# Kernel optimization log

Measured on AMD Instinct MI355X. Metric: run time of the kernel, lower is better.

Reference implementation:

```python
import jax, jax.numpy as jnp
import numpy as np

N, E, C, RB, H = 10000, 160000, 64, 8, 64
AVG_NEIGH = 16.0


def _sph(v):
    # component-normalized real spherical harmonics l=1,2,3 of unit vectors v [E,3]
    x, y, z = v[..., 0], v[..., 1], v[..., 2]
    s3, s5, s15 = 3.0 ** 0.5, 5.0 ** 0.5, 15.0 ** 0.5
    y1 = s3 * jnp.stack([x, y, z], -1)  # [E,3]
    y2 = jnp.stack([
        s15 * x * y,
        s15 * y * z,
        0.5 * s5 * (3.0 * z * z - 1.0),
        s15 * x * z,
        0.5 * s15 * (x * x - y * y),
    ], -1)  # [E,5]
    c1 = (35.0 / 8.0) ** 0.5
    c2 = 105.0 ** 0.5
    c3 = (21.0 / 8.0) ** 0.5
    c4 = (7.0 ** 0.5) / 2.0
    y3 = jnp.stack([
        c1 * y * (3.0 * x * x - y * y),
        c2 * x * y * z,
        c3 * y * (5.0 * z * z - 1.0),
        c4 * z * (5.0 * z * z - 3.0),
        c3 * x * (5.0 * z * z - 1.0),
        0.5 * c2 * z * (x * x - y * y),
        c1 * x * (x * x - y * y),
    ], -1)  # [E,7]
    return y1, y2, y3


def setup_inputs() -> dict:
    key = jax.random.key(0)
    ks = jax.random.split(key, 12)
    inp = {
        'vectors': jax.random.normal(ks[0], (E, 3), jnp.float32),
        'node_feats': jax.random.normal(ks[1], (N, C), jnp.float32),
        'radial_embedding': jax.random.normal(ks[2], (E, RB), jnp.float32),
        'W_up': jax.random.normal(ks[3], (C, C), jnp.float32) / np.sqrt(C),
        'mlp_w1': jax.random.normal(ks[4], (RB, H), jnp.float32) / np.sqrt(RB),
        'mlp_w2': jax.random.normal(ks[5], (H, H), jnp.float32) / np.sqrt(H),
        'mlp_w3': jax.random.normal(ks[6], (H, H), jnp.float32) / np.sqrt(H),
        'mlp_w4': jax.random.normal(ks[7], (H, 4 * C), jnp.float32) / np.sqrt(H),
        'W_down': jax.random.normal(ks[8], (4, C, C), jnp.float32) / np.sqrt(C),
        'senders': jax.random.randint(ks[9], (E,), 0, N, jnp.int32),
        'receivers': jax.random.randint(ks[10], (E,), 0, N, jnp.int32),
    }
    return inp


def reference(vectors, node_feats, radial_embedding, W_up, mlp_w1, mlp_w2, mlp_w3, mlp_w4, W_down, senders, receivers):
    n = node_feats.shape[0]
    # linear_up (scalars: plain channel mixing)
    x = node_feats @ W_up                                   # [N,C]
    sf = x[senders]                                         # [E,C] gather
    u = vectors / (jnp.linalg.norm(vectors, axis=-1, keepdims=True) + 1e-12)
    y1, y2, y3 = _sph(u)
    # radial MLP -> per-irrep mixing weights [E, 4C]
    h = jax.nn.silu(radial_embedding @ mlp_w1)
    h = jax.nn.silu(h @ mlp_w2)
    h = jax.nn.silu(h @ mlp_w3)
    mix = h @ mlp_w4
    m0, m1, m2, m3 = jnp.split(mix, 4, axis=-1)             # each [E,C]
    # tensor product of Cx0e with Y_l -> Cx(l), scaled by radial mix
    msg0 = sf * m0                                          # [E,C]
    msg1 = (sf * m1)[:, :, None] * y1[:, None, :]           # [E,C,3]
    msg2 = (sf * m2)[:, :, None] * y2[:, None, :]           # [E,C,5]
    msg3 = (sf * m3)[:, :, None] * y3[:, None, :]           # [E,C,7]
    inv = 1.0 / jnp.sqrt(jnp.asarray(AVG_NEIGH, msg0.dtype))
    seg = lambda m: jax.ops.segment_sum(m, receivers, num_segments=n) * inv
    o0, o1, o2, o3 = seg(msg0), seg(msg1), seg(msg2), seg(msg3)
    # linear_down: per-l channel mixing
    o0 = o0 @ W_down[0]
    o1 = jnp.einsum('ncm,cd->ndm', o1, W_down[1])
    o2 = jnp.einsum('ncm,cd->ndm', o2, W_down[2])
    o3 = jnp.einsum('ncm,cd->ndm', o3, W_down[3])
    return jnp.concatenate([o0, o1.reshape(n, -1), o2.reshape(n, -1), o3.reshape(n, -1)], axis=-1)  # [N, 16C]
```

## Files before the change

### kernel.cpp

```cpp
#include <hip/hip_runtime.h>
#include <math.h>

#define CC 64
typedef _Float16 f16;
typedef _Float16 half8_t __attribute__((ext_vector_type(8)));
typedef float f32x4 __attribute__((ext_vector_type(4)));

__device__ __forceinline__ float silu_f(float v) {
    return v / (1.0f + __expf(-v));
}

__global__ void k_up(const float* __restrict__ nf, const float* __restrict__ Wup,
                     float* __restrict__ x, int N) {
    int tid = blockIdx.x * blockDim.x + threadIdx.x;
    if (tid >= N * CC) return;
    int n = tid >> 6;
    int j = tid & 63;
    const float* nfr = nf + (size_t)n * CC;
    float acc = 0.f;
#pragma unroll
    for (int k = 0; k < CC; ++k) acc += nfr[k] * Wup[k * CC + j];
    x[tid] = acc;
}

__global__ void k_wt(const float* __restrict__ w1, const float* __restrict__ w2,
                     const float* __restrict__ w3, const float* __restrict__ w4,
                     const float* __restrict__ Wd,
                     f16* __restrict__ wT1, f16* __restrict__ wT2,
                     f16* __restrict__ wT3, f16* __restrict__ wT4,
                     float* __restrict__ wpack) {
    int i = blockIdx.x * 256 + threadIdx.x;
    if (i < 2048) {
        int n = i >> 5, k = i & 31;
        wT1[i] = (k < 8) ? (f16)w1[k * 64 + n] : (f16)0.f;
    } else if (i < 6144) {
        int j = i - 2048; int n = j >> 6, k = j & 63;
        wT2[j] = (f16)w2[k * 64 + n];
    } else if (i < 10240) {
        int j = i - 6144; int n = j >> 6, k = j & 63;
        wT3[j] = (f16)w3[k * 64 + n];
    } else if (i < 26624) {
        int j = i - 10240; int l = j >> 12; int r = j & 4095;
        int n = r >> 6, k = r & 63;
        wT4[j] = (f16)w4[k * 256 + l * 64 + n];
    } else if (i < 43008) {
        int j = i - 26624;
        int pos = j >> 2;
        int comp = j & 3;
        wpack[j] = 0.25f * Wd[comp * 4096 + pos];
    }
}

__global__ void k_hist(const int* __restrict__ rcv, int* __restrict__ cnt, int E) {
    int e = blockIdx.x * blockDim.x + threadIdx.x;
    if (e < E) atomicAdd(&cnt[rcv[e]], 1);
}

__global__ __launch_bounds__(1024) void k_scan(const int* __restrict__ cnt,
        int* __restrict__ off, int* __restrict__ cur, int N) {
    __shared__ int wsum[16];
    int t = threadIdx.x;
    int wave = t >> 6, lane = t & 63;
    int per = (N + 1023) >> 10;
    int i0 = t * per;
    int s = 0;
    for (int j = 0; j < per; ++j) {
        int i = i0 + j;
        if (i < N) s += cnt[i];
    }
    int sc = s;
#pragma unroll
    for (int d = 1; d < 64; d <<= 1) {
        int u = __shfl_up(sc, d, 64);
        if (lane >= d) sc += u;
    }
    if (lane == 63) wsum[wave] = sc;
    __syncthreads();
    if (wave == 0) {
        int v = (lane < 16) ? wsum[lane] : 0;
        int s2 = v;
#pragma unroll
        for (int d = 1; d < 16; d <<= 1) {
            int u = __shfl_up(s2, d, 64);
            if (lane >= d) s2 += u;
        }
        if (lane < 16) wsum[lane] = s2;
    }
    __syncthreads();
    int base = ((wave > 0) ? wsum[wave - 1] : 0) + (sc - s);
    int run = base;
    for (int j = 0; j < per; ++j) {
        int i = i0 + j;
        if (i < N) { off[i] = run; cur[i] = run; run += cnt[i]; }
    }
    if (t == 1023) off[N] = run;
}

__global__ void k_fill(const int* __restrict__ rcv, const int* __restrict__ snd,
                       const float* __restrict__ vec, int* __restrict__ cur,
                       int* __restrict__ eid, int* __restrict__ sndp,
                       float* __restrict__ yb, int E) {
    int e = blockIdx.x * blockDim.x + threadIdx.x;
    if (e >= E) return;
    int p = atomicAdd(&cur[rcv[e]], 1);
    eid[p] = e;
    sndp[p] = snd[e];

    float vx = vec[(size_t)e * 3 + 0];
    float vy = vec[(size_t)e * 3 + 1];
    float vz = vec[(size_t)e * 3 + 2];
    float nrm = sqrtf(vx * vx + vy * vy + vz * vz) + 1e-12f;
    float rinv = 1.0f / nrm;
    float ux = vx * rinv, uy = vy * rinv, uz = vz * rinv;

    const float s3 = 1.7320508075688772f;
    const float s5 = 2.2360679774997896f;
    const float s15 = 3.8729833462074170f;
    const float c1 = 2.0916500663351889f;
    const float c2 = 10.246950765959598f;
    const float c3 = 1.6201851746019651f;
    const float c4 = 1.3228756555322954f;

    float zz = uz * uz, xx = ux * ux, yy = uy * uy;
    float4 r0 = {1.0f, s3 * ux, s3 * uy, s3 * uz};
    float4 r1 = {s15 * ux * uy, s15 * uy * uz, 0.5f * s5 * (3.f * zz - 1.f),
                 s15 * ux * uz};
    float4 r2 = {0.5f * s15 * (xx - yy), c1 * uy * (3.f * xx - yy),
                 c2 * ux * uy * uz, c3 * uy * (5.f * zz - 1.f)};
    float4 r3 = {c4 * uz * (5.f * zz - 3.f), c3 * ux * (5.f * zz - 1.f),
                 0.5f * c2 * uz * (xx - yy), c1 * ux * (xx - yy)};
    float* yr = yb + (size_t)p * 16;
    *(float4*)(yr + 0)  = r0;
    *(float4*)(yr + 4)  = r1;
    *(float4*)(yr + 8)  = r2;
    *(float4*)(yr + 12) = r3;
}

__global__ __launch_bounds__(256) void k_mlp(const float* __restrict__ rad,
        const f16* __restrict__ wT1, const f16* __restrict__ wT2,
        const f16* __restrict__ wT3, const f16* __restrict__ wT4,
        const int* __restrict__ eid, const int* __restrict__ sndp,
        const float* __restrict__ x, f16* __restrict__ mixp, int E) {
    __shared__ f16 act[128][72];

    int t = threadIdx.x;
    int e0 = blockIdx.x * 128;
    int lane = t & 63;
    int wid = t >> 6;
    int m0 = wid * 32;
    int fm = lane & 15;
    int q  = lane >> 4;

    const half8_t hz = {0, 0, 0, 0, 0, 0, 0, 0};

    float4 sfa[4], sfb[4];
#pragma unroll
    for (int it = 0; it < 4; ++it) {
        int row = (lane >> 3) + it * 8;
        int ci = e0 + m0 + row;
        int s = (ci < E) ? sndp[ci] : 0;
        const float* xr = x + (size_t)s * 64 + (lane & 7) * 8;
        sfa[it] = *(const float4*)xr;
        sfb[it] = *(const float4*)(xr + 4);
    }

    half8_t a0 = hz, a1 = hz;
    if (q == 0) {
        int ci0 = e0 + m0 + fm;
        if (ci0 < E) {
            int e = eid[ci0];
            float4 p0 = *(const float4*)(rad + (size_t)e * 8);
            float4 p1 = *(const float4*)(rad + (size_t)e * 8 + 4);
            a0 = (half8_t){(f16)p0.x, (f16)p0.y, (f16)p0.z, (f16)p0.w,
                           (f16)p1.x, (f16)p1.y, (f16)p1.z, (f16)p1.w};
        }
        int ci1 = e0 + m0 + 16 + fm;
        if (ci1 < E) {
            int e = eid[ci1];
            float4 p0 = *(const float4*)(rad + (size_t)e * 8);
            float4 p1 = *(const float4*)(rad + (size_t)e * 8 + 4);
            a1 = (half8_t){(f16)p0.x, (f16)p0.y, (f16)p0.z, (f16)p0.w,
                           (f16)p1.x, (f16)p1.y, (f16)p1.z, (f16)p1.w};
        }
    }
#pragma unroll
    for (int nt = 0; nt < 4; ++nt) {
        half8_t b = *(const half8_t*)(wT1 + ((nt * 16 + fm) << 5) + q * 8);
        f32x4 c0 = {0.f, 0.f, 0.f, 0.f};
        c0 = __builtin_amdgcn_mfma_f32_16x16x32_f16(a0, b, c0, 0, 0, 0);
        f32x4 c1 = {0.f, 0.f, 0.f, 0.f};
        c1 = __builtin_amdgcn_mfma_f32_16x16x32_f16(a1, b, c1, 0, 0, 0);
#pragma unroll
        for (int r = 0; r < 4; ++r) {
            act[m0 + q * 4 + r][nt * 16 + fm]      = (f16)silu_f(c0[r]);
            act[m0 + 16 + q * 4 + r][nt * 16 + fm] = (f16)silu_f(c1[r]);
        }
    }

    auto loadA = [&](int mbase, int kc) -> half8_t {
        return *(const half8_t*)&act[mbase + fm][kc + q * 8];
    };

    const f16* wts[2] = {wT2, wT3};
#pragma unroll
    for (int L = 0; L < 2; ++L) {
        const f16* wT = wts[L];
        half8_t a00 = loadA(m0, 0),      a01 = loadA(m0, 32);
        half8_t a10 = loadA(m0 + 16, 0), a11 = loadA(m0 + 16, 32);
#pragma unroll
        for (int nt = 0; nt < 4; ++nt) {
            const f16* wr = wT + ((nt * 16 + fm) << 6);
            half8_t b0 = *(const half8_t*)(wr + q * 8);
            half8_t b1 = *(const half8_t*)(wr + 32 + q * 8);
            f32x4 c0 = {0.f, 0.f, 0.f, 0.f};
            c0 = __builtin_amdgcn_mfma_f32_16x16x32_f16(a00, b0, c0, 0, 0, 0);
            c0 = __builtin_amdgcn_mfma_f32_16x16x32_f16(a01, b1, c0, 0, 0, 0);
            f32x4 c1 = {0.f, 0.f, 0.f, 0.f};
            c1 = __builtin_amdgcn_mfma_f32_16x16x32_f16(a10, b0, c1, 0, 0, 0);
            c1 = __builtin_amdgcn_mfma_f32_16x16x32_f16(a11, b1, c1, 0, 0, 0);
#pragma unroll
            for (int r = 0; r < 4; ++r) {
                act[m0 + q * 4 + r][nt * 16 + fm]      = (f16)silu_f(c0[r]);
                act[m0 + 16 + q * 4 + r][nt * 16 + fm] = (f16)silu_f(c1[r]);
            }
        }
    }

    half8_t A00 = loadA(m0, 0),      A01 = loadA(m0, 32);
    half8_t A10 = loadA(m0 + 16, 0), A11 = loadA(m0 + 16, 32);

#pragma unroll
    for (int l = 0; l < 4; ++l) {
        const f16* wT = wT4 + (l << 12);
#pragma unroll
        for (int nt = 0; nt < 4; ++nt) {
            const f16* wr = wT + ((nt * 16 + fm) << 6);
            half8_t b0 = *(const half8_t*)(wr + q * 8);
            half8_t b1 = *(const half8_t*)(wr + 32 + q * 8);
            f32x4 c0 = {0.f, 0.f, 0.f, 0.f};
            c0 = __builtin_amdgcn_mfma_f32_16x16x32_f16(A00, b0, c0, 0, 0, 0);
            c0 = __builtin_amdgcn_mfma_f32_16x16x32_f16(A01, b1, c0, 0, 0, 0);
            f32x4 c1 = {0.f, 0.f, 0.f, 0.f};
            c1 = __builtin_amdgcn_mfma_f32_16x16x32_f16(A10, b0, c1, 0, 0, 0);
            c1 = __builtin_amdgcn_mfma_f32_16x16x32_f16(A11, b1, c1, 0, 0, 0);
#pragma unroll
            for (int r = 0; r < 4; ++r) {
                act[m0 + q * 4 + r][nt * 16 + fm]      = (f16)c0[r];
                act[m0 + 16 + q * 4 + r][nt * 16 + fm] = (f16)c1[r];
            }
        }
#pragma unroll
        for (int it = 0; it < 4; ++it) {
            int row = (lane >> 3) + it * 8;
            int ci = e0 + m0 + row;
            if (ci < E) {
                half8_t v = *(const half8_t*)&act[m0 + row][(lane & 7) * 8];
                half8_t w;
                w[0] = (f16)((float)v[0] * sfa[it].x);
                w[1] = (f16)((float)v[1] * sfa[it].y);
                w[2] = (f16)((float)v[2] * sfa[it].z);
                w[3] = (f16)((float)v[3] * sfa[it].w);
                w[4] = (f16)((float)v[4] * sfb[it].x);
                w[5] = (f16)((float)v[5] * sfb[it].y);
                w[6] = (f16)((float)v[6] * sfb[it].z);
                w[7] = (f16)((float)v[7] * sfb[it].w);
                *(half8_t*)&mixp[(size_t)ci * 256 + l * 64 + (lane & 7) * 8] = w;
            }
        }
    }
}

__global__ __launch_bounds__(256) void k_gather(
        const f16* __restrict__ mixp, const float* __restrict__ yb,
        const int* __restrict__ off, const f32x4* __restrict__ wpack,
        float* __restrict__ out, int N) {
    __shared__ float sbuf[4][64 * 20];
    __shared__ float ybs[4][16][16];
    int wv = threadIdx.x >> 6;
    int lane = threadIdx.x & 63;
    int n = blockIdx.x * 4 + wv;
    if (n >= N) return;

    float o[16];
#pragma unroll
    for (int i = 0; i < 16; ++i) o[i] = 0.f;

    auto process = [&](int i, int j) {
        const float* yr = &ybs[wv][j][0];
        f32x4 A  = *(const f32x4*)(yr + 0);
        f32x4 B  = *(const f32x4*)(yr + 4);
        f32x4 Cv = *(const f32x4*)(yr + 8);
        f32x4 D  = *(const f32x4*)(yr + 12);
        const f16* mr = mixp + (size_t)i * 256;
        float t0 = (float)mr[lane];
        float t1 = (float)mr[64 + lane];
        float t2 = (float)mr[128 + lane];
        float t3 = (float)mr[192 + lane];
        o[0]  += t0;
        o[1]  += t1 * A.y;
        o[2]  += t1 * A.z;
        o[3]  += t1 * A.w;
        o[4]  += t2 * B.x;
        o[5]  += t2 * B.y;
        o[6]  += t2 * B.z;
        o[7]  += t2 * B.w;
        o[8]  += t2 * Cv.x;
        o[9]  += t3 * Cv.y;
        o[10] += t3 * Cv.z;
        o[11] += t3 * Cv.w;
        o[12] += t3 * D.x;
        o[13] += t3 * D.y;
        o[14] += t3 * D.z;
        o[15] += t3 * D.w;
    };

    int beg = off[n], end = off[n + 1];
    for (int cb = beg; cb < end; cb += 16) {
        int m = end - cb; if (m > 16) m = 16;
        if (lane < m * 4) {
            f32x4 v = *(const f32x4*)(yb + (size_t)cb * 16 + lane * 4);
            *(f32x4*)&ybs[wv][lane >> 2][(lane & 3) * 4] = v;
        }
        int j = 0;
        for (; j + 1 < m; j += 2) { process(cb + j, j); process(cb + j + 1, j + 1); }
        if (j < m) process(cb + j, j);
    }

    float* sw = sbuf[wv];
#pragma unroll
    for (int a = 0; a < 4; ++a) {
        f32x4 vq = {o[4 * a + 0], o[4 * a + 1], o[4 * a + 2], o[4 * a + 3]};
        *(f32x4*)&sw[lane * 20 + 4 * a] = vq;
    }

    f32x4 dA = {0.f, 0.f, 0.f, 0.f}, dB = dA, dC = dA, dD = dA;
#pragma unroll 2
    for (int c = 0; c < 64; ++c) {
        f32x4 q0 = *(const f32x4*)&sw[c * 20 + 0];
        f32x4 q1 = *(const f32x4*)&sw[c * 20 + 4];
        f32x4 q2 = *(const f32x4*)&sw[c * 20 + 8];
        f32x4 q3 = *(const f32x4*)&sw[c * 20 + 12];
        f32x4 wp = wpack[c * 64 + lane];
        f32x4 wA = {wp.x, wp.y, wp.y, wp.y};
        f32x4 wC4 = {wp.z, wp.w, wp.w, wp.w};
        dA += q0 * wA;
        dB += q1 * wp.z;
        dC += q2 * wC4;
        dD += q3 * wp.w;
    }

    float* outr = out + (size_t)n * 1024;
    outr[lane] = dA[0];
#pragma unroll
    for (int m = 0; m < 3; ++m) outr[64 + lane * 3 + m] = dA[1 + m];
    outr[256 + lane * 5 + 0] = dB[0];
    outr[256 + lane * 5 + 1] = dB[1];
    outr[256 + lane * 5 + 2] = dB[2];
    outr[256 + lane * 5 + 3] = dB[3];
    outr[256 + lane * 5 + 4] = dC[0];
    outr[576 + lane * 7 + 0] = dC[1];
    outr[576 + lane * 7 + 1] = dC[2];
    outr[576 + lane * 7 + 2] = dC[3];
    outr[576 + lane * 7 + 3] = dD[0];
    outr[576 + lane * 7 + 4] = dD[1];
    outr[576 + lane * 7 + 5] = dD[2];
    outr[576 + lane * 7 + 6] = dD[3];
}

extern "C" void kernel_launch(void* const* d_in, const int* in_sizes, int n_in,
                              void* d_out, int out_size, void* d_ws, size_t ws_size,
                              hipStream_t stream) {
    const float* vectors    = (const float*)d_in[0];
    const float* node_feats = (const float*)d_in[1];
    const float* radial     = (const float*)d_in[2];
    const float* W_up       = (const float*)d_in[3];
    const float* w1         = (const float*)d_in[4];
    const float* w2         = (const float*)d_in[5];
    const float* w3         = (const float*)d_in[6];
    const float* w4         = (const float*)d_in[7];
    const float* Wd         = (const float*)d_in[8];
    const int*   snd        = (const int*)d_in[9];
    const int*   rcv        = (const int*)d_in[10];
    float* out = (float*)d_out;

    int E = in_sizes[9];
    int N = in_sizes[1] / CC;

    f16*   wT1   = (f16*)d_ws;
    f16*   wT2   = wT1 + 2048;
    f16*   wT3   = wT2 + 4096;
    f16*   wT4   = wT3 + 4096;
    float* wpack = (float*)(wT4 + 16384);
    float* x     = wpack + 16384;
    float* yb    = x + (size_t)N * 64;
    f16*   mixp  = (f16*)(yb + (size_t)E * 16);
    int*   cnt   = (int*)(mixp + (size_t)E * 256);
    int*   off   = cnt + N;
    int*   cur   = off + (N + 1);
    int*   eid   = cur + N;
    int*   sndp  = eid + E;

    hipMemsetAsync(cnt, 0, (size_t)N * sizeof(int), stream);

    k_wt<<<(43008 + 255) / 256, 256, 0, stream>>>(w1, w2, w3, w4, Wd,
                                                  wT1, wT2, wT3, wT4, wpack);
    k_up<<<(N * CC + 255) / 256, 256, 0, stream>>>(node_feats, W_up, x, N);
    k_hist<<<(E + 255) / 256, 256, 0, stream>>>(rcv, cnt, E);
    k_scan<<<1, 1024, 0, stream>>>(cnt, off, cur, N);
    k_fill<<<(E + 255) / 256, 256, 0, stream>>>(rcv, snd, vectors, cur, eid, sndp, yb, E);
    k_mlp<<<(E + 127) / 128, 256, 0, stream>>>(radial, wT1, wT2, wT3, wT4,
                                               eid, sndp, x, mixp, E);
    k_gather<<<(N + 3) / 4, 256, 0, stream>>>(mixp, yb, off,
                                              (const f32x4*)wpack, out, N);
}
```

Before: 225.6 us.

## Merge preprocessing kernels into one launch and halve MLP tile per block

Three small preprocessing kernels (linear-up, weight transpose/pack, receiver histogram) are combined into one kernel that dispatches on block index, removing two launches and their gaps. The radial-MLP kernel now processes 64 edges per block (16 per wave) instead of 128, halving shared memory and registers per block to raise occupancy and the number of blocks. In exchange, each B-fragment weight load from global now feeds only one MFMA tile instead of two, so weight traffic per edge doubles.

New measurement: 242.0 us. 7.3% more time.

```diff
diff --git a/kernel.cpp b/kernel.cpp
--- a/kernel.cpp
+++ b/kernel.cpp
@@ -10,50 +10,53 @@
     return v / (1.0f + __expf(-v));
 }
 
-__global__ void k_up(const float* __restrict__ nf, const float* __restrict__ Wup,
-                     float* __restrict__ x, int N) {
-    int tid = blockIdx.x * blockDim.x + threadIdx.x;
-    if (tid >= N * CC) return;
-    int n = tid >> 6;
-    int j = tid & 63;
-    const float* nfr = nf + (size_t)n * CC;
-    float acc = 0.f;
-#pragma unroll
-    for (int k = 0; k < CC; ++k) acc += nfr[k] * Wup[k * CC + j];
-    x[tid] = acc;
-}
-
-__global__ void k_wt(const float* __restrict__ w1, const float* __restrict__ w2,
-                     const float* __restrict__ w3, const float* __restrict__ w4,
-                     const float* __restrict__ Wd,
-                     f16* __restrict__ wT1, f16* __restrict__ wT2,
-                     f16* __restrict__ wT3, f16* __restrict__ wT4,
-                     float* __restrict__ wpack) {
-    int i = blockIdx.x * 256 + threadIdx.x;
-    if (i < 2048) {
-        int n = i >> 5, k = i & 31;
-        wT1[i] = (k < 8) ? (f16)w1[k * 64 + n] : (f16)0.f;
-    } else if (i < 6144) {
-        int j = i - 2048; int n = j >> 6, k = j & 63;
-        wT2[j] = (f16)w2[k * 64 + n];
-    } else if (i < 10240) {
-        int j = i - 6144; int n = j >> 6, k = j & 63;
-        wT3[j] = (f16)w3[k * 64 + n];
-    } else if (i < 26624) {
-        int j = i - 10240; int l = j >> 12; int r = j & 4095;
-        int n = r >> 6, k = r & 63;
-        wT4[j] = (f16)w4[k * 256 + l * 64 + n];
-    } else if (i < 43008) {
-        int j = i - 26624;
-        int pos = j >> 2;
-        int comp = j & 3;
-        wpack[j] = 0.25f * Wd[comp * 4096 + pos];
-    }
-}
-
-__global__ void k_hist(const int* __restrict__ rcv, int* __restrict__ cnt, int E) {
-    int e = blockIdx.x * blockDim.x + threadIdx.x;
-    if (e < E) atomicAdd(&cnt[rcv[e]], 1);
+__global__ __launch_bounds__(256) void k_pre(
+        const float* __restrict__ nf, const float* __restrict__ Wup,
+        float* __restrict__ x, int N,
+        const float* __restrict__ w1, const float* __restrict__ w2,
+        const float* __restrict__ w3, const float* __restrict__ w4,
+        const float* __restrict__ Wd,
+        f16* __restrict__ wT1, f16* __restrict__ wT2,
+        f16* __restrict__ wT3, f16* __restrict__ wT4,
+        float* __restrict__ wpack,
+        const int* __restrict__ rcv, int* __restrict__ cnt, int E) {
+    int nb_up = (N * CC + 255) >> 8;
+    int b = blockIdx.x;
+    if (b < nb_up) {
+        int tid = b * 256 + threadIdx.x;
+        if (tid >= N * CC) return;
+        int n = tid >> 6;
+        int j = tid & 63;
+        const float* nfr = nf + (size_t)n * CC;
+        float acc = 0.f;
+#pragma unroll
+        for (int k = 0; k < CC; ++k) acc += nfr[k] * Wup[k * CC + j];
+        x[tid] = acc;
+    } else if (b < nb_up + 168) {
+        int i = (b - nb_up) * 256 + threadIdx.x;
+        if (i < 2048) {
+            int n = i >> 5, k = i & 31;
+            wT1[i] = (k < 8) ? (f16)w1[k * 64 + n] : (f16)0.f;
+        } else if (i < 6144) {
+            int j = i - 2048; int n = j >> 6, k = j & 63;
+            wT2[j] = (f16)w2[k * 64 + n];
+        } else if (i < 10240) {
+            int j = i - 6144; int n = j >> 6, k = j & 63;
+            wT3[j] = (f16)w3[k * 64 + n];
+        } else if (i < 26624) {
+            int j = i - 10240; int l = j >> 12; int r = j & 4095;
+            int n = r >> 6, k = r & 63;
+            wT4[j] = (f16)w4[k * 256 + l * 64 + n];
+        } else if (i < 43008) {
+            int j = i - 26624;
+            int pos = j >> 2;
+            int comp = j & 3;
+            wpack[j] = 0.25f * Wd[comp * 4096 + pos];
+        }
+    } else {
+        int e = (b - nb_up - 168) * 256 + threadIdx.x;
+        if (e < E) atomicAdd(&cnt[rcv[e]], 1);
+    }
 }
 
 __global__ __launch_bounds__(1024) void k_scan(const int* __restrict__ cnt,
@@ -141,21 +144,21 @@
         const f16* __restrict__ wT3, const f16* __restrict__ wT4,
         const int* __restrict__ eid, const int* __restrict__ sndp,
         const float* __restrict__ x, f16* __restrict__ mixp, int E) {
-    __shared__ f16 act[128][72];
+    __shared__ f16 act[64][72];
 
     int t = threadIdx.x;
-    int e0 = blockIdx.x * 128;
+    int e0 = blockIdx.x * 64;
     int lane = t & 63;
     int wid = t >> 6;
-    int m0 = wid * 32;
+    int m0 = wid * 16;
     int fm = lane & 15;
     int q  = lane >> 4;
 
     const half8_t hz = {0, 0, 0, 0, 0, 0, 0, 0};
 
-    float4 sfa[4], sfb[4];
-#pragma unroll
-    for (int it = 0; it < 4; ++it) {
+    float4 sfa[2], sfb[2];
+#pragma unroll
+    for (int it = 0; it < 2; ++it) {
         int row = (lane >> 3) + it * 8;
         int ci = e0 + m0 + row;
         int s = (ci < E) ? sndp[ci] : 0;
@@ -164,7 +167,7 @@
         sfb[it] = *(const float4*)(xr + 4);
     }
 
-    half8_t a0 = hz, a1 = hz;
+    half8_t a0 = hz;
     if (q == 0) {
         int ci0 = e0 + m0 + fm;
         if (ci0 < E) {
@@ -174,39 +177,26 @@
             a0 = (half8_t){(f16)p0.x, (f16)p0.y, (f16)p0.z, (f16)p0.w,
                            (f16)p1.x, (f16)p1.y, (f16)p1.z, (f16)p1.w};
         }
-        int ci1 = e0 + m0 + 16 + fm;
-        if (ci1 < E) {
-            int e = eid[ci1];
-            float4 p0 = *(const float4*)(rad + (size_t)e * 8);
-            float4 p1 = *(const float4*)(rad + (size_t)e * 8 + 4);
-            a1 = (half8_t){(f16)p0.x, (f16)p0.y, (f16)p0.z, (f16)p0.w,
-                           (f16)p1.x, (f16)p1.y, (f16)p1.z, (f16)p1.w};
-        }
     }
 #pragma unroll
     for (int nt = 0; nt < 4; ++nt) {
         half8_t b = *(const half8_t*)(wT1 + ((nt * 16 + fm) << 5) + q * 8);
         f32x4 c0 = {0.f, 0.f, 0.f, 0.f};
         c0 = __builtin_amdgcn_mfma_f32_16x16x32_f16(a0, b, c0, 0, 0, 0);
-        f32x4 c1 = {0.f, 0.f, 0.f, 0.f};
-        c1 = __builtin_amdgcn_mfma_f32_16x16x32_f16(a1, b, c1, 0, 0, 0);
-#pragma unroll
-        for (int r = 0; r < 4; ++r) {
-            act[m0 + q * 4 + r][nt * 16 + fm]      = (f16)silu_f(c0[r]);
-            act[m0 + 16 + q * 4 + r][nt * 16 + fm] = (f16)silu_f(c1[r]);
-        }
-    }
-
-    auto loadA = [&](int mbase, int kc) -> half8_t {
-        return *(const half8_t*)&act[mbase + fm][kc + q * 8];
+#pragma unroll
+        for (int r = 0; r < 4; ++r)
+            act[m0 + q * 4 + r][nt * 16 + fm] = (f16)silu_f(c0[r]);
+    }
+
+    auto loadA = [&](int kc) -> half8_t {
+        return *(const half8_t*)&act[m0 + fm][kc + q * 8];
     };
 
     const f16* wts[2] = {wT2, wT3};
 #pragma unroll
     for (int L = 0; L < 2; ++L) {
         const f16* wT = wts[L];
-        half8_t a00 = loadA(m0, 0),      a01 = loadA(m0, 32);
-        half8_t a10 = loadA(m0 + 16, 0), a11 = loadA(m0 + 16, 32);
+        half8_t a00 = loadA(0), a01 = loadA(32);
 #pragma unroll
         for (int nt = 0; nt < 4; ++nt) {
             const f16* wr = wT + ((nt * 16 + fm) << 6);
@@ -215,19 +205,13 @@
             f32x4 c0 = {0.f, 0.f, 0.f, 0.f};
             c0 = __builtin_amdgcn_mfma_f32_16x16x32_f16(a00, b0, c0, 0, 0, 0);
             c0 = __builtin_amdgcn_mfma_f32_16x16x32_f16(a01, b1, c0, 0, 0, 0);
-            f32x4 c1 = {0.f, 0.f, 0.f, 0.f};
-            c1 = __builtin_amdgcn_mfma_f32_16x16x32_f16(a10, b0, c1, 0, 0, 0);
-            c1 = __builtin_amdgcn_mfma_f32_16x16x32_f16(a11, b1, c1, 0, 0, 0);
-#pragma unroll
-            for (int r = 0; r < 4; ++r) {
-                act[m0 + q * 4 + r][nt * 16 + fm]      = (f16)silu_f(c0[r]);
-                act[m0 + 16 + q * 4 + r][nt * 16 + fm] = (f16)silu_f(c1[r]);
-            }
-        }
-    }
-
-    half8_t A00 = loadA(m0, 0),      A01 = loadA(m0, 32);
-    half8_t A10 = loadA(m0 + 16, 0), A11 = loadA(m0 + 16, 32);
+#pragma unroll
+            for (int r = 0; r < 4; ++r)
+                act[m0 + q * 4 + r][nt * 16 + fm] = (f16)silu_f(c0[r]);
+        }
+    }
+
+    half8_t A00 = loadA(0), A01 = loadA(32);
 
 #pragma unroll
     for (int l = 0; l < 4; ++l) {
@@ -240,17 +224,12 @@
             f32x4 c0 = {0.f, 0.f, 0.f, 0.f};
             c0 = __builtin_amdgcn_mfma_f32_16x16x32_f16(A00, b0, c0, 0, 0, 0);
             c0 = __builtin_amdgcn_mfma_f32_16x16x32_f16(A01, b1, c0, 0, 0, 0);
-            f32x4 c1 = {0.f, 0.f, 0.f, 0.f};
-            c1 = __builtin_amdgcn_mfma_f32_16x16x32_f16(A10, b0, c1, 0, 0, 0);
-            c1 = __builtin_amdgcn_mfma_f32_16x16x32_f16(A11, b1, c1, 0, 0, 0);
-#pragma unroll
-            for (int r = 0; r < 4; ++r) {
-                act[m0 + q * 4 + r][nt * 16 + fm]      = (f16)c0[r];
-                act[m0 + 16 + q * 4 + r][nt * 16 + fm] = (f16)c1[r];
-            }
-        }
-#pragma unroll
-        for (int it = 0; it < 4; ++it) {
+#pragma unroll
+            for (int r = 0; r < 4; ++r)
+                act[m0 + q * 4 + r][nt * 16 + fm] = (f16)c0[r];
+        }
+#pragma unroll
+        for (int it = 0; it < 2; ++it) {
             int row = (lane >> 3) + it * 8;
             int ci = e0 + m0 + row;
             if (ci < E) {
@@ -402,14 +381,15 @@
 
     hipMemsetAsync(cnt, 0, (size_t)N * sizeof(int), stream);
 
-    k_wt<<<(43008 + 255) / 256, 256, 0, stream>>>(w1, w2, w3, w4, Wd,
-                                                  wT1, wT2, wT3, wT4, wpack);
-    k_up<<<(N * CC + 255) / 256, 256, 0, stream>>>(node_feats, W_up, x, N);
-    k_hist<<<(E + 255) / 256, 256, 0, stream>>>(rcv, cnt, E);
+    int nb_up = (N * CC + 255) / 256;
+    int nb_hist = (E + 255) / 256;
+    k_pre<<<nb_up + 168 + nb_hist, 256, 0, stream>>>(
+        node_feats, W_up, x, N, w1, w2, w3, w4, Wd,
+        wT1, wT2, wT3, wT4, wpack, rcv, cnt, E);
     k_scan<<<1, 1024, 0, stream>>>(cnt, off, cur, N);
     k_fill<<<(E + 255) / 256, 256, 0, stream>>>(rcv, snd, vectors, cur, eid, sndp, yb, E);
-    k_mlp<<<(E + 127) / 128, 256, 0, stream>>>(radial, wT1, wT2, wT3, wT4,
-                                               eid, sndp, x, mixp, E);
+    k_mlp<<<(E + 63) / 64, 256, 0, stream>>>(radial, wT1, wT2, wT3, wT4,
+                                             eid, sndp, x, mixp, E);
     k_gather<<<(N + 3) / 4, 256, 0, stream>>>(mixp, yb, off,
                                               (const f32x4*)wpack, out, N);
 }
```
